# Kernel optimization log

Measured on AMD Instinct MI355X. Metric: run time of the kernel, lower is better.

The kernel has to match this reference:

```python
import jax, jax.numpy as jnp
import numpy as np

N = 20000      # total nodes (100 graphs x 200 nodes)
B = 100        # batch_size
PER = 200      # nodes per graph (uniform) -> max_num_nodes
E = 320000     # edges (before self-loops)
F_IN = 32      # num_features
HEADS = 10
OUT = 128      # output_dim
NEG_SLOPE = 0.2  # PyG GATConv default


def setup_inputs() -> dict:
    key = jax.random.key(0)
    ks = jax.random.split(key, 14)
    feats = jax.random.normal(ks[0], (N, F_IN), jnp.float32)
    src = jax.random.randint(ks[1], (E,), 0, N)
    dst = jax.random.randint(ks[2], (E,), 0, N)
    edge_index = jnp.stack([src, dst]).astype(jnp.int32)
    graph_id = jnp.repeat(jnp.arange(B, dtype=jnp.int32), PER)
    batch_num_nodes = jnp.full((B,), PER, jnp.int32)
    s1 = 1.0 / np.sqrt(F_IN)
    s2 = 1.0 / np.sqrt(F_IN * HEADS)
    s3 = 1.0 / np.sqrt(OUT)
    return {
        "feats": feats,
        "edge_index": edge_index,
        "graph_id": graph_id,
        "batch_num_nodes": batch_num_nodes,
        # GATConv 1: in F_IN -> HEADS x F_IN, concat
        "W1": jax.random.normal(ks[3], (F_IN, HEADS * F_IN), jnp.float32) * s1,
        "a1_src": jax.random.normal(ks[4], (HEADS, F_IN), jnp.float32) * s1,
        "a1_dst": jax.random.normal(ks[5], (HEADS, F_IN), jnp.float32) * s1,
        "b1": jnp.zeros((HEADS * F_IN,), jnp.float32),
        "W2": jax.random.normal(ks[6], (HEADS * F_IN, OUT), jnp.float32) * s2,
        "a2_src": jax.random.normal(ks[7], (1, OUT), jnp.float32) * s3,
        "a2_dst": jax.random.normal(ks[8], (1, OUT), jnp.float32) * s3,
        "b2": jnp.zeros((OUT,), jnp.float32),
        # shared fc_g1
        "fc_w": jax.random.normal(ks[9], (OUT, OUT), jnp.float32) * s3,
        "fc_b": jnp.zeros((OUT,), jnp.float32),
    }


def gat_conv(x, src, dst, W, a_src, a_dst, bias, heads, out_dim):
    # x: [N, Fin]; src/dst already include self-loops (PyG default add_self_loops=True)
    n = x.shape[0]
    xw = (x @ W).reshape(n, heads, out_dim)                 # [N,H,F]
    s_src = jnp.einsum('nhf,hf->nh', xw, a_src)             # [N,H]
    s_dst = jnp.einsum('nhf,hf->nh', xw, a_dst)
    e = jax.nn.leaky_relu(s_src[src] + s_dst[dst], NEG_SLOPE)  # [E,H]
    # segment softmax over incoming edges of each destination node
    m = jax.ops.segment_max(e, dst, num_segments=n)         # [N,H]
    ex = jnp.exp(e - m[dst])
    denom = jax.ops.segment_sum(ex, dst, num_segments=n)    # [N,H]
    alpha = ex / jnp.maximum(denom[dst], 1e-16)             # [E,H]
    out = jax.ops.segment_sum(alpha[:, :, None] * xw[src], dst, num_segments=n)  # [N,H,F]
    return out.reshape(n, heads * out_dim) + bias


def reference(feats, edge_index, graph_id, batch_num_nodes,
              W1, a1_src, a1_dst, b1, W2, a2_src, a2_dst, b2, fc_w, fc_b):
    n = feats.shape[0]
    loops = jnp.arange(n, dtype=edge_index.dtype)
    src = jnp.concatenate([edge_index[0], loops])
    dst = jnp.concatenate([edge_index[1], loops])
    x = feats.astype(jnp.float32)
    # dropout layers are identity in eval mode
    x = jax.nn.elu(gat_conv(x, src, dst, W1, a1_src, a1_dst, b1, HEADS, F_IN))
    x = gat_conv(x, src, dst, W2, a2_src, a2_dst, b2, 1, OUT)
    x = jax.nn.relu(x)                                       # [N, OUT]
    # dgl_split: scatter node feats into [B, max_num_nodes, OUT] padded tensor
    cum = jnp.concatenate([jnp.zeros((1,), jnp.int32),
                           jnp.cumsum(batch_num_nodes).astype(jnp.int32)])
    idx = jnp.arange(n, dtype=jnp.int32) - cum[graph_id] + graph_id * PER
    padded = jnp.zeros((B * PER, OUT), x.dtype).at[idx].set(x).reshape(B, PER, OUT)
    out = jax.nn.relu(padded @ fc_w + fc_b)                  # [B, PER, OUT]
    # global max pool per graph, then shared fc_g1 + relu
    pooled = jax.ops.segment_max(x, graph_id, num_segments=B)  # [B, OUT]
    pooled = jax.nn.relu(pooled @ fc_w + fc_b)
    return (out, pooled)
```

## Files before the change

kernel.cpp:

```cpp
#include <hip/hip_runtime.h>

#define N_NODES 20000
#define N_EDGES 320000
#define ETOT    (N_EDGES + N_NODES)
#define HEADS   10
#define F_IN    32
#define C1      (HEADS * F_IN)
#define C2      128
#define NB      100
#define PER     200
#define CAP     96
#define SSTRIDE 12
#define HSTRIDE 328
#define X2STRIDE 136

typedef __attribute__((ext_vector_type(8))) short bf16x8;
typedef __attribute__((ext_vector_type(4))) float floatx4;
typedef _Float16 f16;
typedef _Float16 f16x2 __attribute__((ext_vector_type(2)));
typedef _Float16 f16x4 __attribute__((ext_vector_type(4)));
typedef _Float16 f16x8 __attribute__((ext_vector_type(8)));

static __device__ __forceinline__ unsigned short f2bf(float f) {
    unsigned int u = __float_as_uint(f);
    unsigned int r = (u + 0x7fffu + ((u >> 16) & 1u)) >> 16;
    return (unsigned short)r;
}

#define SCAT_BLOCKS  ((ETOT + 255) / 256)
#define SCORE_BLOCKS ((N_NODES + 63) / 64)
#define W2P_BLOCKS   ((C1 * C2 + 255) / 256)
#define W1P_BLOCKS   ((HEADS * F_IN * F_IN + 255) / 256)
#define FCP_BLOCKS   ((C2 * C2 + 255) / 256)
#define F16_BLOCKS   ((N_NODES * F_IN / 4 + 255) / 256)
__global__ __launch_bounds__(256) void mega_prep_kernel(
        const int* __restrict__ ei, int* __restrict__ cursor, int* __restrict__ csr_src,
        const float* __restrict__ feats, f16* __restrict__ feats16,
        const float* __restrict__ W1, unsigned short* __restrict__ W1p,
        const float* __restrict__ W2, unsigned short* __restrict__ W2p,
        const float* __restrict__ fcw, f16* __restrict__ FCp,
        const float* __restrict__ a1s, const float* __restrict__ a1d,
        float* __restrict__ s_src, float* __restrict__ s_dst) {
    unsigned int b = blockIdx.x;
    if (b < SCAT_BLOCKS) {
        int e = b * 256 + threadIdx.x;
        if (e >= ETOT) return;
        int s, d;
        if (e < N_EDGES) { s = ei[e]; d = ei[N_EDGES + e]; }
        else             { s = e - N_EDGES; d = s; }
        int pos = atomicAdd(&cursor[d], 1);
        csr_src[(size_t)d * CAP + pos] = s;
        return;
    }
    b -= SCAT_BLOCKS;
    if (b < SCORE_BLOCKS) {
        __shared__ __align__(16) float A[64 * F_IN];
        __shared__ float Ws[C1], Wd[C1];
        int t = threadIdx.x;
        for (int o = t; o < C1; o += 256) {
            int k = o & 31, h = o >> 5;
            float ss = 0.f, dd = 0.f;
#pragma unroll
            for (int f = 0; f < F_IN; f++) {
                float wv = W1[k * C1 + h * 32 + f];
                ss += wv * a1s[h * 32 + f];
                dd += wv * a1d[h * 32 + f];
            }
            Ws[k * HEADS + h] = ss;
            Wd[k * HEADS + h] = dd;
        }
        int n0 = b * 64;
        int nrows = min(64, N_NODES - n0);
        const float4* fs = (const float4*)(feats + (size_t)n0 * F_IN);
        float4* Af = (float4*)A;
        for (int i = t; i < nrows * 8; i += 256) Af[i] = fs[i];
        __syncthreads();
        for (int o = t; o < nrows * HEADS; o += 256) {
            int nl = o / HEADS, h = o - nl * HEADS;
            const float* ar = A + nl * F_IN;
            float ss = 0.f, dd = 0.f;
#pragma unroll
            for (int k = 0; k < F_IN; k++) {
                float av = ar[k];
                ss += av * Ws[k * HEADS + h];
                dd += av * Wd[k * HEADS + h];
            }
            s_src[(size_t)(n0 + nl) * SSTRIDE + h] = ss;
            s_dst[(size_t)(n0 + nl) * SSTRIDE + h] = dd;
        }
        return;
    }
    b -= SCORE_BLOCKS;
    if (b < W2P_BLOCKS) {
        int o = b * 256 + threadIdx.x;
        if (o >= C1 * C2) return;
        int j    = o & 7;
        int lane = (o >> 3) & 63;
        int ct   = (o >> 9) & 7;
        int kb   = o >> 12;
        int k = kb * 32 + (lane >> 4) * 8 + j;
        int n = ct * 16 + (lane & 15);
        W2p[o] = f2bf(W2[k * C2 + n]);
        return;
    }
    b -= W2P_BLOCKS;
    if (b < W1P_BLOCKS) {
        int o = b * 256 + threadIdx.x;
        if (o >= HEADS * F_IN * F_IN) return;
        int j    = o & 7;
        int lane = (o >> 3) & 63;
        int ct   = (o >> 9) & 1;
        int h    = o >> 10;
        int k = (lane >> 4) * 8 + j;
        int f = ct * 16 + (lane & 15);
        W1p[o] = f2bf(W1[k * C1 + h * 32 + f]);
        return;
    }
    b -= W1P_BLOCKS;
    if (b < FCP_BLOCKS) {
        int o = b * 256 + threadIdx.x;
        if (o >= C2 * C2) return;
        int j    = o & 7;
        int lane = (o >> 3) & 63;
        int ct   = (o >> 9) & 7;
        int kb   = o >> 12;
        int k = kb * 32 + (lane >> 4) * 8 + j;
        int n = ct * 16 + (lane & 15);
        FCp[o] = (f16)fcw[k * C2 + n];
        return;
    }
    b -= FCP_BLOCKS;
    {
        int o = b * 256 + threadIdx.x;
        if (o < N_NODES * F_IN / 4) {
            float4 v = ((const float4*)feats)[o];
            f16* d = feats16 + 4 * o;
            d[0] = (f16)v.x; d[1] = (f16)v.y; d[2] = (f16)v.z; d[3] = (f16)v.w;
        }
    }
}

__global__ __launch_bounds__(512) void agg1h1g2_kernel(
        const f16* __restrict__ feats16, const float* __restrict__ s_src,
        const float* __restrict__ s_dst, const int* __restrict__ deg_arr,
        const int* __restrict__ csr_src,
        const unsigned short* __restrict__ W1p, const float* __restrict__ b1,
        const unsigned short* __restrict__ W2p,
        const float* __restrict__ a_src, const float* __restrict__ a_dst,
        f16* __restrict__ xw2h, float* __restrict__ s_src2, float* __restrict__ s_dst2) {
    union Smem {
        struct { f16 P[16][HEADS * 32]; int S[16][32]; } p1;
        unsigned short H[16 * HSTRIDE];
    };
    __shared__ __align__(16) Smem u;
    __shared__ __align__(16) unsigned short G[16 * HSTRIDE];
    __shared__ float redS[8][16], redD[8][16];

    int tid   = threadIdx.x;
    int wslot = tid >> 6;
    int lane  = tid & 63;
    int r     = tid >> 5;
    int l     = tid & 31;
    int row0  = blockIdx.x * 16;
    f16* P = u.p1.P[r];
    int* S = u.p1.S[r];
    const f16x2 ones = {(f16)1.f, (f16)1.f};
    const char* fb = (const char*)feats16 + 2 * l;

    {
        int n = row0 + r;
        int beg = n * CAP, deg = deg_arr[n];
        const float* sdp = s_dst + (size_t)n * SSTRIDE;
        float sd[10];
        {
            float4 v0 = *(const float4*)(sdp);
            float4 v1 = *(const float4*)(sdp + 4);
            float2 v2 = *(const float2*)(sdp + 8);
            sd[0]=v0.x; sd[1]=v0.y; sd[2]=v0.z; sd[3]=v0.w;
            sd[4]=v1.x; sd[5]=v1.y; sd[6]=v1.z; sd[7]=v1.w;
            sd[8]=v2.x; sd[9]=v2.y;
        }
        float g[10], la[10];
#pragma unroll
        for (int h = 0; h < 10; h++) { g[h] = 0.f; la[h] = 0.f; }

        for (int c0 = 0; c0 < deg; c0 += 32) {
            int dc = min(deg - c0, 32);
            bool act = l < dc;
            int s_e = csr_src[beg + c0 + min(l, dc - 1)];
            const float* ssp = s_src + (size_t)s_e * SSTRIDE;
            float ss[10];
            {
                float4 v0 = *(const float4*)(ssp);
                float4 v1 = *(const float4*)(ssp + 4);
                float2 v2 = *(const float2*)(ssp + 8);
                ss[0]=v0.x; ss[1]=v0.y; ss[2]=v0.z; ss[3]=v0.w;
                ss[4]=v1.x; ss[5]=v1.y; ss[6]=v1.z; ss[7]=v1.w;
                ss[8]=v2.x; ss[9]=v2.y;
            }
            float p[10];
#pragma unroll
            for (int h = 0; h < 10; h++) {
                float e0 = ss[h] + sd[h];
                e0 = (e0 >= 0.f) ? e0 : 0.2f * e0;
                p[h] = act ? __expf(e0) : 0.f;
            }
            S[l] = s_e << 6;
#pragma unroll
            for (int h = 0; h < 10; h++) P[h * 32 + l] = (f16)p[h];
            asm volatile("s_waitcnt lgkmcnt(0)" ::: "memory");

#pragma unroll
            for (int i = 0; i < 32; i += 4) {
                int4 ss4 = *(const int4*)&S[i];
                f16x2 v01, v23;
                v01.x = *(const f16*)(fb + ss4.x);
                v01.y = *(const f16*)(fb + ss4.y);
                v23.x = *(const f16*)(fb + ss4.z);
                v23.y = *(const f16*)(fb + ss4.w);
#pragma unroll
                for (int h = 0; h < 10; h++) {
                    f16x4 pp = *(const f16x4*)&P[h * 32 + i];
                    f16x2 p01 = {pp[0], pp[1]};
                    f16x2 p23 = {pp[2], pp[3]};
                    g[h]  = __builtin_amdgcn_fdot2(p01, v01, g[h], false);
                    g[h]  = __builtin_amdgcn_fdot2(p23, v23, g[h], false);
                    la[h] = __builtin_amdgcn_fdot2(p01, ones, la[h], false);
                    la[h] = __builtin_amdgcn_fdot2(p23, ones, la[h], false);
                }
            }
            asm volatile("s_waitcnt lgkmcnt(0)" ::: "memory");
        }
        unsigned short* gr = &G[r * HSTRIDE + l];
#pragma unroll
        for (int h = 0; h < 10; h++)
            gr[h * 32] = f2bf(g[h] / fmaxf(la[h], 1e-16f));
    }
    __syncthreads();

    int quad = lane >> 4, col = lane & 15;
    for (int h = wslot; h < 10; h += 8) {
        bf16x8 a = *(const bf16x8*)&G[col * HSTRIDE + h * 32 + quad * 8];
        bf16x8 bA = ((const bf16x8*)W1p)[(h * 2 + 0) * 64 + lane];
        bf16x8 bB = ((const bf16x8*)W1p)[(h * 2 + 1) * 64 + lane];
        floatx4 z = {0.f, 0.f, 0.f, 0.f};
        floatx4 c0 = __builtin_amdgcn_mfma_f32_16x16x32_bf16(a, bA, z, 0, 0, 0);
        floatx4 c1 = __builtin_amdgcn_mfma_f32_16x16x32_bf16(a, bB, z, 0, 0, 0);
        float bias0 = b1[h * 32 + col];
        float bias1 = b1[h * 32 + 16 + col];
#pragma unroll
        for (int reg = 0; reg < 4; reg++) {
            int rr = quad * 4 + reg;
            float o0 = c0[reg] + bias0;
            float o1 = c1[reg] + bias1;
            o0 = (o0 > 0.f) ? o0 : (__expf(o0) - 1.f);
            o1 = (o1 > 0.f) ? o1 : (__expf(o1) - 1.f);
            u.H[rr * HSTRIDE + h * 32 + col]      = f2bf(o0);
            u.H[rr * HSTRIDE + h * 32 + 16 + col] = f2bf(o1);
        }
    }
    __syncthreads();

    floatx4 acc = {0.f, 0.f, 0.f, 0.f};
    const bf16x8* pb = (const bf16x8*)W2p;
#pragma unroll
    for (int kb = 0; kb < 10; kb++) {
        bf16x8 a = *(const bf16x8*)&u.H[col * HSTRIDE + kb * 32 + quad * 8];
        bf16x8 b = pb[(kb * 8 + wslot) * 64 + lane];
        acc = __builtin_amdgcn_mfma_f32_16x16x32_bf16(a, b, acc, 0, 0, 0);
    }
    float asv = a_src[wslot * 16 + col];
    float adv = a_dst[wslot * 16 + col];
#pragma unroll
    for (int reg = 0; reg < 4; reg++) {
        int row = row0 + quad * 4 + reg;
        float v = acc[reg];
        xw2h[(size_t)row * C2 + wslot * 16 + col] = (f16)v;
        float vs = v * asv, vd = v * adv;
#pragma unroll
        for (int off = 8; off >= 1; off >>= 1) {
            vs += __shfl_xor(vs, off);
            vd += __shfl_xor(vd, off);
        }
        if (col == 0) { redS[wslot][quad * 4 + reg] = vs; redD[wslot][quad * 4 + reg] = vd; }
    }
    __syncthreads();
    if (wslot == 0) {
        if (lane < 16) {
            float s = 0.f;
#pragma unroll
            for (int w2 = 0; w2 < 8; w2++) s += redS[w2][lane];
            s_src2[row0 + lane] = s;
        } else if (lane < 32) {
            int r2 = lane - 16;
            float d = 0.f;
#pragma unroll
            for (int w2 = 0; w2 < 8; w2++) d += redD[w2][r2];
            s_dst2[row0 + r2] = d;
        }
    }
}

__global__ __launch_bounds__(512) void agg2fc_kernel(
        const f16* __restrict__ xw2h, const float* __restrict__ s_src2,
        const float* __restrict__ s_dst2, const int* __restrict__ deg_arr,
        const int* __restrict__ csr_src, const float* __restrict__ b2,
        const f16* __restrict__ FCp, const float* __restrict__ fcb,
        float* __restrict__ out, int* __restrict__ pooledi) {
    __shared__ __align__(16) int2 shE[16][32];
    __shared__ __align__(16) f16 X[16 * X2STRIDE];
    int tid   = threadIdx.x;
    int wslot = tid >> 6;
    int lane  = tid & 63;
    int r     = tid >> 5;
    int l     = tid & 31;
    int row0  = blockIdx.x * 16;
    int2* E = shE[r];
    const char* xb = (const char*)xw2h + 8 * l;

    {
        int n = row0 + r;
        int beg = n * CAP, deg = deg_arr[n];
        float sd = s_dst2[n];
        float ldn = 0.f, a0 = 0.f, a1 = 0.f, a2 = 0.f, a3 = 0.f;

        for (int c0 = 0; c0 < deg; c0 += 32) {
            int dc = min(deg - c0, 32);
            bool act = l < dc;
            int s_e = csr_src[beg + c0 + min(l, dc - 1)];
            float e = s_src2[s_e] + sd;
            e = (e >= 0.f) ? e : 0.2f * e;
            float p = act ? __expf(e) : 0.f;
            float su = p;
#pragma unroll
            for (int off = 16; off >= 1; off >>= 1) su += __shfl_xor(su, off);
            ldn += su;

            E[l] = make_int2(s_e << 8, __float_as_int(p));
            asm volatile("s_waitcnt lgkmcnt(0)" ::: "memory");

#pragma unroll
            for (int i = 0; i < 32; i += 4) {
                int4 e01 = *(const int4*)&E[i];
                int4 e23 = *(const int4*)&E[i + 2];
                f16x4 v0 = *(const f16x4*)(xb + e01.x);
                f16x4 v1 = *(const f16x4*)(xb + e01.z);
                f16x4 v2 = *(const f16x4*)(xb + e23.x);
                f16x4 v3 = *(const f16x4*)(xb + e23.z);
                float p0 = __int_as_float(e01.y), p1 = __int_as_float(e01.w);
                float p2 = __int_as_float(e23.y), p3 = __int_as_float(e23.w);
                a0 += p0 * (float)v0[0] + p1 * (float)v1[0] + p2 * (float)v2[0] + p3 * (float)v3[0];
                a1 += p0 * (float)v0[1] + p1 * (float)v1[1] + p2 * (float)v2[1] + p3 * (float)v3[1];
                a2 += p0 * (float)v0[2] + p1 * (float)v1[2] + p2 * (float)v2[2] + p3 * (float)v3[2];
                a3 += p0 * (float)v0[3] + p1 * (float)v1[3] + p2 * (float)v2[3] + p3 * (float)v3[3];
            }
            asm volatile("s_waitcnt lgkmcnt(0)" ::: "memory");
        }

        float linv = 1.f / fmaxf(ldn, 1e-16f);
        float4 bb = *(const float4*)(b2 + 4 * l);
        f16x4 o;
        o[0] = (f16)fmaxf(a0 * linv + bb.x, 0.f);
        o[1] = (f16)fmaxf(a1 * linv + bb.y, 0.f);
        o[2] = (f16)fmaxf(a2 * linv + bb.z, 0.f);
        o[3] = (f16)fmaxf(a3 * linv + bb.w, 0.f);
        *(f16x4*)&X[r * X2STRIDE + 4 * l] = o;
    }
    __syncthreads();

    int quad = lane >> 4, col = lane & 15;
    floatx4 acc = {0.f, 0.f, 0.f, 0.f};
    const f16x8* pb = (const f16x8*)FCp;
#pragma unroll
    for (int kb = 0; kb < 4; kb++) {
        f16x8 a = *(const f16x8*)&X[col * X2STRIDE + kb * 32 + quad * 8];
        f16x8 b = pb[(kb * 8 + wslot) * 64 + lane];
        acc = __builtin_amdgcn_mfma_f32_16x16x32_f16(a, b, acc, 0, 0, 0);
    }
    float bias = fcb[wslot * 16 + col];
#pragma unroll
    for (int reg = 0; reg < 4; reg++) {
        int row = row0 + quad * 4 + reg;
        out[(size_t)row * C2 + wslot * 16 + col] = fmaxf(acc[reg] + bias, 0.f);
    }

    if (tid < C2) {
        int c = tid;
        int gA = row0 / PER;
        int gB = (row0 + 15) / PER;
        float mA = 0.f, mB = 0.f;
#pragma unroll
        for (int rr = 0; rr < 16; rr++) {
            float v = (float)X[rr * X2STRIDE + c];
            if ((row0 + rr) / PER == gA) mA = fmaxf(mA, v);
            else                         mB = fmaxf(mB, v);
        }
        atomicMax(&pooledi[gA * C2 + c], __float_as_int(mA));
        if (gB != gA) atomicMax(&pooledi[gB * C2 + c], __float_as_int(mB));
    }
}

__global__ void poolfc_kernel(const int* __restrict__ pooledi, const float* __restrict__ fcw,
                              const float* __restrict__ fcb, float* __restrict__ outp) {
    __shared__ float mx[C2];
    int g = blockIdx.x, t = threadIdx.x;
    mx[t] = __int_as_float(pooledi[g * C2 + t]);
    __syncthreads();
    float acc = 0.f;
    for (int k = 0; k < C2; k++) acc += mx[k] * fcw[k * C2 + t];
    outp[g * C2 + t] = fmaxf(acc + fcb[t], 0.f);
}

extern "C" void kernel_launch(void* const* d_in, const int* in_sizes, int n_in,
                              void* d_out, int out_size, void* d_ws, size_t ws_size,
                              hipStream_t stream) {
    const float* feats = (const float*)d_in[0];
    const int*   ei    = (const int*)d_in[1];
    const float* W1  = (const float*)d_in[4];
    const float* a1s = (const float*)d_in[5];
    const float* a1d = (const float*)d_in[6];
    const float* b1  = (const float*)d_in[7];
    const float* W2  = (const float*)d_in[8];
    const float* a2s = (const float*)d_in[9];
    const float* a2d = (const float*)d_in[10];
    const float* b2  = (const float*)d_in[11];
    const float* fcw = (const float*)d_in[12];
    const float* fcb = (const float*)d_in[13];

    float* out_main = (float*)d_out;
    float* out_pool = (float*)d_out + (size_t)N_NODES * C2;

    char* p = (char*)d_ws;
    auto alloc = [&](size_t bytes) {
        char* r = p;
        p += (bytes + 255) & ~(size_t)255;
        return r;
    };
    unsigned short* W2p  = (unsigned short*)alloc(sizeof(short) * C1 * C2);
    unsigned short* W1p  = (unsigned short*)alloc(sizeof(short) * HEADS * F_IN * F_IN);
    f16*   FCp     = (f16*)alloc(sizeof(f16) * C2 * C2);
    f16*   feats16 = (f16*)alloc(sizeof(f16) * (size_t)N_NODES * F_IN);
    f16*   xw2h    = (f16*)alloc(sizeof(f16) * (size_t)N_NODES * C2);
    float* s1s    = (float*)alloc(sizeof(float) * N_NODES * SSTRIDE);
    float* s1d    = (float*)alloc(sizeof(float) * N_NODES * SSTRIDE);
    float* s2s    = (float*)alloc(sizeof(float) * N_NODES);
    float* s2d    = (float*)alloc(sizeof(float) * N_NODES);
    const int NZ = N_NODES + NB * C2;
    int* zeros   = (int*)alloc(sizeof(int) * NZ);
    int* cursor  = zeros;
    int* pooledi = zeros + N_NODES;
    int* csr_src = (int*)alloc(sizeof(int) * N_NODES * CAP);

    hipMemsetAsync(zeros, 0, sizeof(int) * NZ, stream);

    mega_prep_kernel<<<SCAT_BLOCKS + SCORE_BLOCKS + W2P_BLOCKS + W1P_BLOCKS + FCP_BLOCKS + F16_BLOCKS,
                       256, 0, stream>>>(
        ei, cursor, csr_src, feats, feats16, W1, W1p, W2, W2p, fcw, FCp,
        a1s, a1d, s1s, s1d);

    agg1h1g2_kernel<<<1250, 512, 0, stream>>>(feats16, s1s, s1d, cursor, csr_src,
                                              W1p, b1, W2p, a2s, a2d, xw2h, s2s, s2d);
    agg2fc_kernel<<<1250, 512, 0, stream>>>(xw2h, s2s, s2d, cursor, csr_src, b2,
                                            FCp, fcb, out_main, pooledi);
    poolfc_kernel<<<NB, C2, 0, stream>>>(pooledi, fcw, fcb, out_pool);
}
```

Measured before the change: 158.9 us.

## Fold pool-FC into agg2 via last-block counters; replace memset with fold/zero kernel

The pooled fc_g1 computation moves into the tail of agg2fc_kernel. Per-graph completion counters let the last of the 13 contributing blocks read the max-pooled vector and compute the FC, which removes the separate poolfc launch. The hipMemset is replaced by a small kernel that zeroes the counters and also precomputes the W1·a1 attention folds once, instead of in every score block of mega_prep. This saves launches and redundant per-block recomputation, but adds a dependent kernel, thread fences and atomics.

```diff
diff --git a/kernel.cpp b/kernel.cpp
--- a/kernel.cpp
+++ b/kernel.cpp
@@ -13,6 +13,7 @@
 #define SSTRIDE 12
 #define HSTRIDE 328
 #define X2STRIDE 136
+#define NZCNT   (N_NODES + NB * C2 + NB)
 
 typedef __attribute__((ext_vector_type(8))) short bf16x8;
 typedef __attribute__((ext_vector_type(4))) float floatx4;
@@ -25,6 +26,35 @@
     unsigned int u = __float_as_uint(f);
     unsigned int r = (u + 0x7fffu + ((u >> 16) & 1u)) >> 16;
     return (unsigned short)r;
+}
+
+__global__ __launch_bounds__(256) void fold_zero_kernel(
+        const float* __restrict__ W1, const float* __restrict__ a1s,
+        const float* __restrict__ a1d, float* __restrict__ wsF,
+        float* __restrict__ wdF, int* __restrict__ zeros) {
+    unsigned int b = blockIdx.x;
+    int t = threadIdx.x;
+    if (b == 0) {
+        for (int o = t; o < C1; o += 256) {
+            int k = o & 31, h = o >> 5;
+            float ss = 0.f, dd = 0.f;
+#pragma unroll
+            for (int f = 0; f < F_IN; f++) {
+                float wv = W1[k * C1 + h * 32 + f];
+                ss += wv * a1s[h * 32 + f];
+                dd += wv * a1d[h * 32 + f];
+            }
+            wsF[k * HEADS + h] = ss;
+            wdF[k * HEADS + h] = dd;
+        }
+        return;
+    }
+    int i = (b - 1) * 256 + t;
+    const int n4 = (NZCNT + 3) / 4;
+    if (i < n4) {
+        int4 z = {0, 0, 0, 0};
+        ((int4*)zeros)[i] = z;
+    }
 }
 
 #define SCAT_BLOCKS  ((ETOT + 255) / 256)
@@ -39,7 +69,7 @@
         const float* __restrict__ W1, unsigned short* __restrict__ W1p,
         const float* __restrict__ W2, unsigned short* __restrict__ W2p,
         const float* __restrict__ fcw, f16* __restrict__ FCp,
-        const float* __restrict__ a1s, const float* __restrict__ a1d,
+        const float* __restrict__ wsF, const float* __restrict__ wdF,
         float* __restrict__ s_src, float* __restrict__ s_dst) {
     unsigned int b = blockIdx.x;
     if (b < SCAT_BLOCKS) {
@@ -58,16 +88,8 @@
         __shared__ float Ws[C1], Wd[C1];
         int t = threadIdx.x;
         for (int o = t; o < C1; o += 256) {
-            int k = o & 31, h = o >> 5;
-            float ss = 0.f, dd = 0.f;
-#pragma unroll
-            for (int f = 0; f < F_IN; f++) {
-                float wv = W1[k * C1 + h * 32 + f];
-                ss += wv * a1s[h * 32 + f];
-                dd += wv * a1d[h * 32 + f];
-            }
-            Ws[k * HEADS + h] = ss;
-            Wd[k * HEADS + h] = dd;
+            Ws[o] = wsF[o];
+            Wd[o] = wdF[o];
         }
         int n0 = b * 64;
         int nrows = min(64, N_NODES - n0);
@@ -306,9 +328,14 @@
         const float* __restrict__ s_dst2, const int* __restrict__ deg_arr,
         const int* __restrict__ csr_src, const float* __restrict__ b2,
         const f16* __restrict__ FCp, const float* __restrict__ fcb,
-        float* __restrict__ out, int* __restrict__ pooledi) {
+        const float* __restrict__ fcw,
+        float* __restrict__ out, float* __restrict__ outp,
+        int* __restrict__ pooledi, int* __restrict__ done) {
     __shared__ __align__(16) int2 shE[16][32];
     __shared__ __align__(16) f16 X[16 * X2STRIDE];
+    __shared__ float pool_mx[C2];
+    __shared__ float pool_part[4][C2];
+    __shared__ int win_s[2];
     int tid   = threadIdx.x;
     int wslot = tid >> 6;
     int lane  = tid & 63;
@@ -384,10 +411,10 @@
         out[(size_t)row * C2 + wslot * 16 + col] = fmaxf(acc[reg] + bias, 0.f);
     }
 
+    int gA = row0 / PER;
+    int gB = (row0 + 15) / PER;
     if (tid < C2) {
         int c = tid;
-        int gA = row0 / PER;
-        int gB = (row0 + 15) / PER;
         float mA = 0.f, mB = 0.f;
 #pragma unroll
         for (int rr = 0; rr < 16; rr++) {
@@ -398,17 +425,36 @@
         atomicMax(&pooledi[gA * C2 + c], __float_as_int(mA));
         if (gB != gA) atomicMax(&pooledi[gB * C2 + c], __float_as_int(mB));
     }
-}
-
-__global__ void poolfc_kernel(const int* __restrict__ pooledi, const float* __restrict__ fcw,
-                              const float* __restrict__ fcb, float* __restrict__ outp) {
-    __shared__ float mx[C2];
-    int g = blockIdx.x, t = threadIdx.x;
-    mx[t] = __int_as_float(pooledi[g * C2 + t]);
     __syncthreads();
-    float acc = 0.f;
-    for (int k = 0; k < C2; k++) acc += mx[k] * fcw[k * C2 + t];
-    outp[g * C2 + t] = fmaxf(acc + fcb[t], 0.f);
+
+    if (tid == 0) {
+        __threadfence();
+        int tA = atomicAdd(&done[gA], 1);
+        int wA = (tA == 12);
+        int wB = 0;
+        if (gB != gA) { int tB = atomicAdd(&done[gB], 1); wB = (tB == 12); }
+        win_s[0] = wA; win_s[1] = wB;
+    }
+    __syncthreads();
+
+    auto pool_fc = [&](int g2) {
+        int t = tid;
+        if (t < C2)
+            pool_mx[t] = __int_as_float(atomicMax(&pooledi[g2 * C2 + t], 0));
+        __syncthreads();
+        int pc = t & (C2 - 1), piece = t >> 7;
+        float acc2 = 0.f;
+        const float* fw = fcw + (size_t)(piece * 32) * C2 + pc;
+        const float* mp = pool_mx + piece * 32;
+        for (int k = 0; k < 32; k++) acc2 += mp[k] * fw[(size_t)k * C2];
+        pool_part[piece][pc] = acc2;
+        __syncthreads();
+        if (piece == 0)
+            outp[(size_t)g2 * C2 + pc] = fmaxf(pool_part[0][pc] + pool_part[1][pc] +
+                                               pool_part[2][pc] + pool_part[3][pc] + fcb[pc], 0.f);
+    };
+    if (win_s[0]) pool_fc(gA);
+    if (win_s[1]) pool_fc(gB);
 }
 
 extern "C" void kernel_launch(void* const* d_in, const int* in_sizes, int n_in,
@@ -445,22 +491,25 @@
     float* s1d    = (float*)alloc(sizeof(float) * N_NODES * SSTRIDE);
     float* s2s    = (float*)alloc(sizeof(float) * N_NODES);
     float* s2d    = (float*)alloc(sizeof(float) * N_NODES);
-    const int NZ = N_NODES + NB * C2;
-    int* zeros   = (int*)alloc(sizeof(int) * NZ);
+    float* wsF    = (float*)alloc(sizeof(float) * C1);
+    float* wdF    = (float*)alloc(sizeof(float) * C1);
+    int* zeros   = (int*)alloc(sizeof(int) * ((NZCNT + 63) & ~63));
     int* cursor  = zeros;
     int* pooledi = zeros + N_NODES;
+    int* done    = zeros + N_NODES + NB * C2;
     int* csr_src = (int*)alloc(sizeof(int) * N_NODES * CAP);
 
-    hipMemsetAsync(zeros, 0, sizeof(int) * NZ, stream);
+    fold_zero_kernel<<<1 + (((NZCNT + 3) / 4 + 255) / 256), 256, 0, stream>>>(
+        W1, a1s, a1d, wsF, wdF, zeros);
 
     mega_prep_kernel<<<SCAT_BLOCKS + SCORE_BLOCKS + W2P_BLOCKS + W1P_BLOCKS + FCP_BLOCKS + F16_BLOCKS,
                        256, 0, stream>>>(
         ei, cursor, csr_src, feats, feats16, W1, W1p, W2, W2p, fcw, FCp,
-        a1s, a1d, s1s, s1d);
+        wsF, wdF, s1s, s1d);
 
     agg1h1g2_kernel<<<1250, 512, 0, stream>>>(feats16, s1s, s1d, cursor, csr_src,
                                               W1p, b1, W2p, a2s, a2d, xw2h, s2s, s2d);
     agg2fc_kernel<<<1250, 512, 0, stream>>>(xw2h, s2s, s2d, cursor, csr_src, b2,
-                                            FCp, fcb, out_main, pooledi);
-    poolfc_kernel<<<NB, C2, 0, stream>>>(pooledi, fcw, fcb, out_pool);
+                                            FCp, fcb, fcw, out_main, out_pool,
+                                            pooledi, done);
 }
```

Result: slower. 192.6 us (+21.2%).
